# Performance work log

Hardware: AMD Instinct MI355X
Metric: run time of the kernel (lower is better)

Reference implementation:

```python
import jax, jax.numpy as jnp
import numpy as np

NEG = -1e30  # log-space 'zero' (avoids -inf NaN issues under jit)
EPS = 1e-7   # keras.backend.epsilon()


def _ctc_loss(y_true, y_pred):
    # y_true: [B, L] int labels in [0, C-1), y_pred: [B, T, C] softmax probs.
    # Keras ctc_batch_cost: logits = log(y_pred + eps), then tf.nn.ctc_loss
    # (which applies log_softmax internally), blank = C - 1.
    B, T, C = y_pred.shape
    L = y_true.shape[1]
    S = 2 * L + 1
    blank = C - 1

    logp = jax.nn.log_softmax(jnp.log(y_pred + EPS), axis=-1)  # [B, T, C]

    # Extended label sequence: blank, l1, blank, l2, ..., blank  -> [B, S]
    ext = jnp.full((B, S), blank, dtype=y_true.dtype).at[:, 1::2].set(y_true)
    lp_ext = jnp.take_along_axis(logp, ext[:, None, :].astype(jnp.int32), axis=2)  # [B, T, S]

    # skip transition s-2 -> s allowed iff ext[s] != blank and ext[s] != ext[s-2]
    ext_m2 = jnp.concatenate([jnp.full((B, 2), blank, ext.dtype), ext[:, :-2]], axis=1)
    allow_skip = (ext != blank) & (ext != ext_m2)
    allow_skip = allow_skip.at[:, :2].set(False)

    # alpha init at t=0
    alpha = jnp.full((B, S), NEG, dtype=logp.dtype)
    alpha = alpha.at[:, 0].set(lp_ext[:, 0, 0]).at[:, 1].set(lp_ext[:, 0, 1])

    neg1 = jnp.full((B, 1), NEG, dtype=logp.dtype)
    neg2 = jnp.full((B, 2), NEG, dtype=logp.dtype)

    def step(a, lp_t):
        prev1 = jnp.concatenate([neg1, a[:, :-1]], axis=1)
        prev2 = jnp.concatenate([neg2, a[:, :-2]], axis=1)
        acc = jnp.logaddexp(a, prev1)
        acc = jnp.where(allow_skip, jnp.logaddexp(acc, prev2), acc)
        return acc + lp_t, None

    lp_seq = jnp.transpose(lp_ext, (1, 0, 2))[1:]  # [T-1, B, S]
    alpha, _ = jax.lax.scan(step, alpha, lp_seq)

    loss = -jnp.logaddexp(alpha[:, -1], alpha[:, -2])  # [B]
    return loss[:, None]  # [B, 1] like keras ctc_batch_cost


def setup_inputs() -> dict:
    key = jax.random.key(0)
    k1, k2 = jax.random.split(key)
    B, T, C, L = 1024, 256, 128, 64
    y_true = jax.random.randint(k1, (B, L), 0, C - 1, dtype=jnp.int32)
    y_pred = jax.random.uniform(k2, (B, T, C), dtype=jnp.float32, minval=1e-4, maxval=1.0)
    return {"y_true": y_true, "y_pred": y_pred}


def reference(y_true, y_pred):
    return _ctc_loss(y_true, y_pred)
```

## Files before the change

kernel.cpp:

```cpp
#include <hip/hip_runtime.h>
#include <math.h>

#define BATCH 1024
#define TT    256
#define CC    128
#define LL    64
#define EPSV  (1e-7f)

typedef float f32x4 __attribute__((ext_vector_type(4)));
typedef __fp16 fp16x2 __attribute__((ext_vector_type(2)));

template <int CTRL>
__device__ __forceinline__ float dpp0(float x) {
    return __int_as_float(__builtin_amdgcn_update_dpp(0, __float_as_int(x), CTRL, 0xF, 0xF, true));
}
template <int CTRL>
__device__ __forceinline__ float dppS(float x) {
    return __int_as_float(__builtin_amdgcn_update_dpp(__float_as_int(x), __float_as_int(x), CTRL, 0xF, 0xF, false));
}
__device__ __forceinline__ float rol1_f(float x) {
    return __int_as_float(__builtin_amdgcn_update_dpp(__float_as_int(x), __float_as_int(x), 0x134, 0xF, 0xF, false));
}
__device__ __forceinline__ int rol1_i(int x) {
    return __builtin_amdgcn_update_dpp(x, x, 0x134, 0xF, 0xF, false);
}
__device__ __forceinline__ float rdlane(float x, int l) {
    return __int_as_float(__builtin_amdgcn_readlane(__float_as_int(x), l));
}
__device__ __forceinline__ float wave_max_bcast(float m) {
    m = fmaxf(m, dppS<0x111>(m));
    m = fmaxf(m, dppS<0x112>(m));
    m = fmaxf(m, dppS<0x114>(m));
    m = fmaxf(m, dppS<0x118>(m));
    m = fmaxf(m, dppS<0x142>(m));
    m = fmaxf(m, dppS<0x143>(m));
    return rdlane(m, 63);
}
__device__ __forceinline__ int pkrtz(float a, float b) {
    fp16x2 h = __builtin_amdgcn_cvt_pkrtz(a, b);
    int r; __builtin_memcpy(&r, &h, 4);
    return r;
}
__device__ __forceinline__ float h2f(unsigned short u) {
    _Float16 h; __builtin_memcpy(&h, &u, 2);
    return (float)h;
}

__global__ __launch_bounds__(512, 8) void ctc_fwd_kernel(const int* __restrict__ y_true,
                                                         const float* __restrict__ y_pred,
                                                         float* __restrict__ out) {
    __shared__ unsigned short qtab[TT][66];
    __shared__ float qblank[TT];
    __shared__ float logZpart[8];
    __shared__ int   chunkCnt[32];
    __shared__ int   doneCnt;

    const int b    = blockIdx.x;
    const int tid  = threadIdx.x;
    const int wv   = tid >> 6;
    const int lane = tid & 63;

    const float* yp = y_pred + (size_t)b * (TT * CC);
    const int lab  = y_true[b * LL + lane];
    const int srcA = lab >> 2;
    const int srcB = 32 + srcA;
    const bool hiPair = (lab & 2) != 0;
    const bool hiHalf = (lab & 1) != 0;

    const int off = ((lane >> 5) << 7) + ((lane & 31) << 2);
    const float* base = yp + off;

    if (tid < 32) chunkCnt[tid] = 0;
    if (tid == 32) doneCnt = 0;
    __syncthreads();

    if (wv > 0) {
        const int sw = wv - 1;
        float zacc = 0.0f;
        f32x4 v[8];
        #pragma unroll
        for (int d = 0; d < 8; ++d) {
            int r2 = sw + 7 * d; r2 = (r2 < 128) ? r2 : 127;
            v[d] = *(const f32x4*)(base + 256 * r2);
        }
        #pragma unroll
        for (int i = 0; i < 19; ++i) {
            const int  r2i   = sw + 7 * i;
            const bool valid = (r2i < 128);
            const int  r2    = valid ? r2i : 127;
            f32x4 x = v[i & 7];
            if (i + 8 < 19) {
                int rn = sw + 7 * (i + 8); rn = (rn < 128) ? rn : 127;
                v[i & 7] = *(const f32x4*)(base + 256 * rn);
            }
            const int tA = 2 * r2, tB = tA + 1;
            float q0 = x[0] + EPSV, q1 = x[1] + EPSV;
            float q2 = x[2] + EPSV, q3 = x[3] + EPSV;
            float s = (q0 + q1) + (q2 + q3);
            s += dpp0<0x111>(s);
            s += dpp0<0x112>(s);
            s += dpp0<0x114>(s);
            s += dpp0<0x118>(s);
            s += dpp0<0x142>(s);
            if (valid) zacc += __logf(s);
            int i01 = pkrtz(q0, q1);
            int i23 = pkrtz(q2, q3);
            int gA01 = __shfl(i01, srcA), gA23 = __shfl(i23, srcA);
            int gB01 = __shfl(i01, srcB), gB23 = __shfl(i23, srcB);
            int sA = hiPair ? gA23 : gA01;
            int sB = hiPair ? gB23 : gB01;
            if (valid) {
                qtab[tA][lane] = (unsigned short)(hiHalf ? ((unsigned)sA >> 16) : (sA & 0xFFFF));
                qtab[tB][lane] = (unsigned short)(hiHalf ? ((unsigned)sB >> 16) : (sB & 0xFFFF));
                if ((lane & 31) == 31) qblank[tA + (lane >> 5)] = q3;
                asm volatile("s_waitcnt lgkmcnt(0)" ::: "memory");
                if (lane == 0) atomicAdd(&chunkCnt[r2 >> 2], 1);
            }
        }
        float z31 = rdlane(zacc, 31), z63 = rdlane(zacc, 63);
        if (lane == 0) {
            logZpart[wv] = z31 + z63;
            asm volatile("s_waitcnt lgkmcnt(0)" ::: "memory");
            atomicAdd(&doneCnt, 1);
        }
    } else {
        const int   labm1 = rol1_i(lab);
        const float mskip = (lane >= 1 && lab != labm1) ? 1.0f : 0.0f;
        const bool  l0 = (lane == 0);

        volatile int* vcnt = chunkCnt;
        while (vcnt[0] < 4) __builtin_amdgcn_s_sleep(1);
        __builtin_amdgcn_sched_barrier(0);

        float a0 = l0 ? qblank[0] : 0.0f;
        float a1 = l0 ? h2f(qtab[0][lane]) : 0.0f;
        float aX = 0.0f;
        int Esum = 0;

        {
            float qb8[8], ql8[8];
            #pragma unroll
            for (int i = 1; i < 8; ++i) { qb8[i] = qblank[i]; ql8[i] = h2f(qtab[i][lane]); }
            #pragma unroll
            for (int i = 1; i < 8; ++i) {
                float nb  = rol1_f(a1);
                float na0 = (a0 + (l0 ? 0.0f : nb)) * qb8[i];
                float na1 = fmaf(mskip, nb, a0 + a1) * ql8[i];
                aX = l0 ? (aX + nb) * qb8[i] : 0.0f;
                a0 = na0; a1 = na1;
            }
            float mall = wave_max_bcast(fmaxf(fmaxf(a0, a1), aX));
            int e = 127 - (int)((__float_as_uint(mall) >> 23) & 0xFF);
            float sc = __uint_as_float((unsigned)(127 + e) << 23);
            a0 *= sc; a1 *= sc; aX *= sc;
            Esum += e;
        }
        for (int c = 1; c < 32; ++c) {
            while (vcnt[c] < 4) __builtin_amdgcn_s_sleep(1);
            __builtin_amdgcn_sched_barrier(0);
            float qb8[8], ql8[8];
            #pragma unroll
            for (int i = 0; i < 8; ++i) {
                const int t = 8 * c + i;
                qb8[i] = qblank[t];
                ql8[i] = h2f(qtab[t][lane]);
            }
            #pragma unroll
            for (int i = 0; i < 8; ++i) {
                float nb  = rol1_f(a1);
                float na0 = (a0 + (l0 ? 0.0f : nb)) * qb8[i];
                float na1 = fmaf(mskip, nb, a0 + a1) * ql8[i];
                aX = l0 ? (aX + nb) * qb8[i] : 0.0f;
                a0 = na0; a1 = na1;
            }
            float mall = wave_max_bcast(fmaxf(fmaxf(a0, a1), aX));
            int e = 127 - (int)((__float_as_uint(mall) >> 23) & 0xFF);
            float sc = __uint_as_float((unsigned)(127 + e) << 23);
            a0 *= sc; a1 *= sc; aX *= sc;
            Esum += e;
        }
        volatile int* vd = &doneCnt;
        while (*vd < 7) __builtin_amdgcn_s_sleep(1);
        __builtin_amdgcn_sched_barrier(0);
        float LZ = 0.0f;
        #pragma unroll
        for (int w = 1; w < 8; ++w) LZ += logZpart[w];
        float a127 = rdlane(a1, 63);
        if (lane == 0) {
            out[b] = LZ + (float)Esum * 0.69314718055994531f - __logf(aX + a127);
        }
    }
}

extern "C" void kernel_launch(void* const* d_in, const int* in_sizes, int n_in,
                              void* d_out, int out_size, void* d_ws, size_t ws_size,
                              hipStream_t stream) {
    const int*   y_true = (const int*)d_in[0];
    const float* y_pred = (const float*)d_in[1];
    float*       out    = (float*)d_out;
    ctc_fwd_kernel<<<BATCH, 512, 0, stream>>>(y_true, y_pred, out);
}
```

Measured before the change: 37.26 us.

## Split warps into direct label gatherers and separate normalizer reducers

Waves 6 and 7 now gather each label's probability and the blank directly from global memory, one half of the time axis each, and publish progress through a per-half counter. Waves 1-5 compute only the per-timestep normalizer. They accumulate mantissa products and exponents instead of taking a log every step. This removes the shuffle-based gather and the per-chunk atomics, and drops the padding on the fp16 table. In exchange the gather does strided scalar loads that re-read lines already fetched by the normalizer waves, and the product of up to 26 mantissas may lose some precision.

```diff
diff --git a/kernel.cpp b/kernel.cpp
--- a/kernel.cpp
+++ b/kernel.cpp
@@ -8,7 +8,6 @@
 #define EPSV  (1e-7f)
 
 typedef float f32x4 __attribute__((ext_vector_type(4)));
-typedef __fp16 fp16x2 __attribute__((ext_vector_type(2)));
 
 template <int CTRL>
 __device__ __forceinline__ float dpp0(float x) {
@@ -36,10 +35,10 @@
     m = fmaxf(m, dppS<0x143>(m));
     return rdlane(m, 63);
 }
-__device__ __forceinline__ int pkrtz(float a, float b) {
-    fp16x2 h = __builtin_amdgcn_cvt_pkrtz(a, b);
-    int r; __builtin_memcpy(&r, &h, 4);
-    return r;
+__device__ __forceinline__ unsigned short f16b(float x) {
+    _Float16 h = (_Float16)x;
+    unsigned short u; __builtin_memcpy(&u, &h, 2);
+    return u;
 }
 __device__ __forceinline__ float h2f(unsigned short u) {
     _Float16 h; __builtin_memcpy(&h, &u, 2);
@@ -49,10 +48,10 @@
 __global__ __launch_bounds__(512, 8) void ctc_fwd_kernel(const int* __restrict__ y_true,
                                                          const float* __restrict__ y_pred,
                                                          float* __restrict__ out) {
-    __shared__ unsigned short qtab[TT][66];
+    __shared__ unsigned short qtab[TT][64];
     __shared__ float qblank[TT];
-    __shared__ float logZpart[8];
-    __shared__ int   chunkCnt[32];
+    __shared__ float logZpart[5];
+    __shared__ int   gatherDone[2];
     __shared__ int   doneCnt;
 
     const int b    = blockIdx.x;
@@ -62,64 +61,69 @@
 
     const float* yp = y_pred + (size_t)b * (TT * CC);
     const int lab  = y_true[b * LL + lane];
-    const int srcA = lab >> 2;
-    const int srcB = 32 + srcA;
-    const bool hiPair = (lab & 2) != 0;
-    const bool hiHalf = (lab & 1) != 0;
-
-    const int off = ((lane >> 5) << 7) + ((lane & 31) << 2);
-    const float* base = yp + off;
-
-    if (tid < 32) chunkCnt[tid] = 0;
-    if (tid == 32) doneCnt = 0;
+
+    if (tid < 2) gatherDone[tid] = 0;
+    if (tid == 2) doneCnt = 0;
     __syncthreads();
 
-    if (wv > 0) {
+    if (wv >= 6) {
+        const int half = (wv == 7) ? 0 : 1;
+        const int t0 = half * 128;
+        float b0 = yp[(size_t)(t0 + lane) * CC + 127];
+        float b1 = yp[(size_t)(t0 + 64 + lane) * CC + 127];
+        qblank[t0 + lane]      = b0 + EPSV;
+        qblank[t0 + 64 + lane] = b1 + EPSV;
+        const float* gp = yp + lab;
+        float val[16];
+        #pragma unroll
+        for (int d = 0; d < 16; ++d) val[d] = gp[(size_t)(t0 + d) * CC];
+        for (int c = 0; c < 16; ++c) {
+            #pragma unroll
+            for (int i = 0; i < 8; ++i) {
+                const int r = 8 * c + i;
+                float x = val[r & 15];
+                if (r + 16 < 128) val[r & 15] = gp[(size_t)(t0 + r + 16) * CC];
+                qtab[t0 + r][lane] = f16b(x + EPSV);
+            }
+            asm volatile("s_waitcnt lgkmcnt(0)" ::: "memory");
+            if (lane == 0) *(volatile int*)&gatherDone[half] = 8 * c + 8;
+        }
+    } else if (wv >= 1) {
         const int sw = wv - 1;
-        float zacc = 0.0f;
+        const int off = ((lane >> 5) << 7) + ((lane & 31) << 2);
+        const float* base = yp + off;
+        float prodM = 1.0f;
+        int   expS  = 0;
         f32x4 v[8];
         #pragma unroll
         for (int d = 0; d < 8; ++d) {
-            int r2 = sw + 7 * d; r2 = (r2 < 128) ? r2 : 127;
+            int r2 = sw + 5 * d; r2 = (r2 < 128) ? r2 : 127;
             v[d] = *(const f32x4*)(base + 256 * r2);
         }
         #pragma unroll
-        for (int i = 0; i < 19; ++i) {
-            const int  r2i   = sw + 7 * i;
+        for (int i = 0; i < 26; ++i) {
+            const int  r2i   = sw + 5 * i;
             const bool valid = (r2i < 128);
-            const int  r2    = valid ? r2i : 127;
             f32x4 x = v[i & 7];
-            if (i + 8 < 19) {
-                int rn = sw + 7 * (i + 8); rn = (rn < 128) ? rn : 127;
+            if (i + 8 < 26) {
+                int rn = sw + 5 * (i + 8); rn = (rn < 128) ? rn : 127;
                 v[i & 7] = *(const f32x4*)(base + 256 * rn);
             }
-            const int tA = 2 * r2, tB = tA + 1;
-            float q0 = x[0] + EPSV, q1 = x[1] + EPSV;
-            float q2 = x[2] + EPSV, q3 = x[3] + EPSV;
-            float s = (q0 + q1) + (q2 + q3);
+            float s = ((x[0] + x[1]) + (x[2] + x[3])) + 4.0f * EPSV;
             s += dpp0<0x111>(s);
             s += dpp0<0x112>(s);
             s += dpp0<0x114>(s);
             s += dpp0<0x118>(s);
             s += dpp0<0x142>(s);
-            if (valid) zacc += __logf(s);
-            int i01 = pkrtz(q0, q1);
-            int i23 = pkrtz(q2, q3);
-            int gA01 = __shfl(i01, srcA), gA23 = __shfl(i23, srcA);
-            int gB01 = __shfl(i01, srcB), gB23 = __shfl(i23, srcB);
-            int sA = hiPair ? gA23 : gA01;
-            int sB = hiPair ? gB23 : gB01;
-            if (valid) {
-                qtab[tA][lane] = (unsigned short)(hiHalf ? ((unsigned)sA >> 16) : (sA & 0xFFFF));
-                qtab[tB][lane] = (unsigned short)(hiHalf ? ((unsigned)sB >> 16) : (sB & 0xFFFF));
-                if ((lane & 31) == 31) qblank[tA + (lane >> 5)] = q3;
-                asm volatile("s_waitcnt lgkmcnt(0)" ::: "memory");
-                if (lane == 0) atomicAdd(&chunkCnt[r2 >> 2], 1);
-            }
-        }
-        float z31 = rdlane(zacc, 31), z63 = rdlane(zacc, 63);
+            unsigned bits = __float_as_uint(s);
+            int   e    = (int)((bits >> 23) & 0xFF) - 127;
+            float mant = __uint_as_float((bits & 0x007FFFFFu) | 0x3F800000u);
+            if (valid) { prodM *= mant; expS += e; }
+        }
+        float zlog = __logf(prodM) + (float)expS * 0.69314718055994531f;
+        float z31 = rdlane(zlog, 31), z63 = rdlane(zlog, 63);
         if (lane == 0) {
-            logZpart[wv] = z31 + z63;
+            logZpart[sw] = z31 + z63;
             asm volatile("s_waitcnt lgkmcnt(0)" ::: "memory");
             atomicAdd(&doneCnt, 1);
         }
@@ -128,10 +132,11 @@
         const float mskip = (lane >= 1 && lab != labm1) ? 1.0f : 0.0f;
         const bool  l0 = (lane == 0);
 
-        volatile int* vcnt = chunkCnt;
-        while (vcnt[0] < 4) __builtin_amdgcn_s_sleep(1);
-        __builtin_amdgcn_sched_barrier(0);
-
+        {
+            volatile int* g = &gatherDone[0];
+            while (*g < 8) __builtin_amdgcn_s_sleep(1);
+            __builtin_amdgcn_sched_barrier(0);
+        }
         float a0 = l0 ? qblank[0] : 0.0f;
         float a1 = l0 ? h2f(qtab[0][lane]) : 0.0f;
         float aX = 0.0f;
@@ -156,7 +161,10 @@
             Esum += e;
         }
         for (int c = 1; c < 32; ++c) {
-            while (vcnt[c] < 4) __builtin_amdgcn_s_sleep(1);
+            const int half = c >> 4;
+            const int need = ((c & 15) + 1) * 8;
+            volatile int* g = &gatherDone[half];
+            while (*g < need) __builtin_amdgcn_s_sleep(1);
             __builtin_amdgcn_sched_barrier(0);
             float qb8[8], ql8[8];
             #pragma unroll
@@ -180,11 +188,11 @@
             Esum += e;
         }
         volatile int* vd = &doneCnt;
-        while (*vd < 7) __builtin_amdgcn_s_sleep(1);
+        while (*vd < 5) __builtin_amdgcn_s_sleep(1);
         __builtin_amdgcn_sched_barrier(0);
         float LZ = 0.0f;
         #pragma unroll
-        for (int w = 1; w < 8; ++w) LZ += logZpart[w];
+        for (int w = 0; w < 5; ++w) LZ += logZpart[w];
         float a127 = rdlane(a1, 63);
         if (lane == 0) {
             out[b] = LZ + (float)Esum * 0.69314718055994531f - __logf(aX + a127);
```

Result: slower. 71.45 us, median of 4 (+91.8%).

## Pack two timesteps per dword in shared table, halve shuffles, defer log

Applied to the files above, without the earlier changes.

The shared label-probability table now holds fp16 values for two adjacent timesteps packed into one 32-bit word, so producers issue one LDS store and the consumer wave one LDS read per timestep pair. The gather is rearranged so each lane does two shuffles instead of four, choosing the source registers by half-wave and label parity. The per-row log of the normaliser is replaced by accumulating exponents and multiplying mantissas, with a single log at the end. Risks are extra select logic and a small change in rounding from the mantissa-product accumulation.

```diff
diff --git a/kernel.cpp b/kernel.cpp
--- a/kernel.cpp
+++ b/kernel.cpp
@@ -49,7 +49,7 @@
 __global__ __launch_bounds__(512, 8) void ctc_fwd_kernel(const int* __restrict__ y_true,
                                                          const float* __restrict__ y_pred,
                                                          float* __restrict__ out) {
-    __shared__ unsigned short qtab[TT][66];
+    __shared__ unsigned qtab32[128][64];
     __shared__ float qblank[TT];
     __shared__ float logZpart[8];
     __shared__ int   chunkCnt[32];
@@ -76,7 +76,8 @@
 
     if (wv > 0) {
         const int sw = wv - 1;
-        float zacc = 0.0f;
+        float prodM = 1.0f;
+        int   expS  = 0;
         f32x4 v[8];
         #pragma unroll
         for (int d = 0; d < 8; ++d) {
@@ -93,7 +94,6 @@
                 int rn = sw + 7 * (i + 8); rn = (rn < 128) ? rn : 127;
                 v[i & 7] = *(const f32x4*)(base + 256 * rn);
             }
-            const int tA = 2 * r2, tB = tA + 1;
             float q0 = x[0] + EPSV, q1 = x[1] + EPSV;
             float q2 = x[2] + EPSV, q3 = x[3] + EPSV;
             float s = (q0 + q1) + (q2 + q3);
@@ -102,22 +102,30 @@
             s += dpp0<0x114>(s);
             s += dpp0<0x118>(s);
             s += dpp0<0x142>(s);
-            if (valid) zacc += __logf(s);
+            unsigned bits = __float_as_uint(s);
+            if (valid) {
+                expS += (int)((bits >> 23) & 0xFF) - 127;
+                prodM *= __uint_as_float((bits & 0x007FFFFFu) | 0x3F800000u);
+            }
             int i01 = pkrtz(q0, q1);
             int i23 = pkrtz(q2, q3);
-            int gA01 = __shfl(i01, srcA), gA23 = __shfl(i23, srcA);
-            int gB01 = __shfl(i01, srcB), gB23 = __shfl(i23, srcB);
-            int sA = hiPair ? gA23 : gA01;
-            int sB = hiPair ? gB23 : gB01;
+            int X = (lane < 32) ? i01 : i23;
+            int Y = (lane < 32) ? i23 : i01;
+            int u = __shfl(X, hiPair ? srcB : srcA);
+            int w = __shfl(Y, hiPair ? srcA : srcB);
+            int sA = hiPair ? w : u;
+            int sB = hiPair ? u : w;
+            unsigned hA = hiHalf ? ((unsigned)sA >> 16) : ((unsigned)sA & 0xFFFF);
+            unsigned hB = hiHalf ? ((unsigned)sB >> 16) : ((unsigned)sB & 0xFFFF);
             if (valid) {
-                qtab[tA][lane] = (unsigned short)(hiHalf ? ((unsigned)sA >> 16) : (sA & 0xFFFF));
-                qtab[tB][lane] = (unsigned short)(hiHalf ? ((unsigned)sB >> 16) : (sB & 0xFFFF));
-                if ((lane & 31) == 31) qblank[tA + (lane >> 5)] = q3;
+                qtab32[r2][lane] = hA | (hB << 16);
+                if ((lane & 31) == 31) qblank[2 * r2 + (lane >> 5)] = q3;
                 asm volatile("s_waitcnt lgkmcnt(0)" ::: "memory");
                 if (lane == 0) atomicAdd(&chunkCnt[r2 >> 2], 1);
             }
         }
-        float z31 = rdlane(zacc, 31), z63 = rdlane(zacc, 63);
+        float zlog = __logf(prodM) + (float)expS * 0.69314718055994531f;
+        float z31 = rdlane(zlog, 31), z63 = rdlane(zlog, 63);
         if (lane == 0) {
             logZpart[wv] = z31 + z63;
             asm volatile("s_waitcnt lgkmcnt(0)" ::: "memory");
@@ -133,14 +141,21 @@
         __builtin_amdgcn_sched_barrier(0);
 
         float a0 = l0 ? qblank[0] : 0.0f;
-        float a1 = l0 ? h2f(qtab[0][lane]) : 0.0f;
+        float a1 = l0 ? h2f((unsigned short)(qtab32[0][lane] & 0xFFFF)) : 0.0f;
         float aX = 0.0f;
         int Esum = 0;
 
         {
+            unsigned q4[4];
+            #pragma unroll
+            for (int j = 0; j < 4; ++j) q4[j] = qtab32[j][lane];
             float qb8[8], ql8[8];
             #pragma unroll
-            for (int i = 1; i < 8; ++i) { qb8[i] = qblank[i]; ql8[i] = h2f(qtab[i][lane]); }
+            for (int i = 1; i < 8; ++i) {
+                qb8[i] = qblank[i];
+                unsigned uu = q4[i >> 1];
+                ql8[i] = h2f((unsigned short)((i & 1) ? (uu >> 16) : (uu & 0xFFFF)));
+            }
             #pragma unroll
             for (int i = 1; i < 8; ++i) {
                 float nb  = rol1_f(a1);
@@ -158,12 +173,15 @@
         for (int c = 1; c < 32; ++c) {
             while (vcnt[c] < 4) __builtin_amdgcn_s_sleep(1);
             __builtin_amdgcn_sched_barrier(0);
+            unsigned q4[4];
+            #pragma unroll
+            for (int j = 0; j < 4; ++j) q4[j] = qtab32[4 * c + j][lane];
             float qb8[8], ql8[8];
             #pragma unroll
             for (int i = 0; i < 8; ++i) {
-                const int t = 8 * c + i;
-                qb8[i] = qblank[t];
-                ql8[i] = h2f(qtab[t][lane]);
+                qb8[i] = qblank[8 * c + i];
+                unsigned uu = q4[i >> 1];
+                ql8[i] = h2f((unsigned short)((i & 1) ? (uu >> 16) : (uu & 0xFFFF)));
             }
             #pragma unroll
             for (int i = 0; i < 8; ++i) {
```

New measurement: 36.50 us. -2.0%, faster.
